# Kernel tuning notes

Measured on AMD Instinct MI355X. Metric: run time of the kernel, lower is better.

Reference implementation:

```python
import jax, jax.numpy as jnp
import numpy as np

MEM, KEY, VAL, DIN, BS, BQ = 1000, 64, 128, 512, 512, 65536


def setup_inputs() -> dict:
    key = jax.random.key(0)
    ks = jax.random.split(key, 20)

    def lin(k, fan_in, shape):
        return (jax.random.normal(k, shape, jnp.float32) / np.sqrt(fan_in)).astype(jnp.float32)

    return {
        "support_x": jax.random.normal(ks[0], (BS, DIN), jnp.float32),
        "support_y": jax.random.normal(ks[1], (BS, VAL), jnp.float32),
        "query_x": jax.random.normal(ks[2], (BQ, DIN), jnp.float32),
        "query_y": jax.random.normal(ks[3], (BQ, 1), jnp.float32),
        # base model: Linear(DIN -> KEY)
        "base_W": lin(ks[4], DIN, (DIN, KEY)),
        "base_b": jnp.zeros((KEY,), jnp.float32),
        # ExternalMemory projections
        "kp_W": lin(ks[5], KEY, (KEY, KEY)),
        "kp_b": jnp.zeros((KEY,), jnp.float32),
        "vp_W": lin(ks[6], VAL, (VAL, VAL)),
        "vp_b": jnp.zeros((VAL,), jnp.float32),
        # memory buffers (randn keys/values like register_buffer(torch.randn))
        "mem_keys": jax.random.normal(ks[7], (MEM, KEY), jnp.float32),
        "mem_values": jax.random.normal(ks[8], (MEM, VAL), jnp.float32),
        # ages: uniform so top-k picks distinct slots deterministically
        "mem_age": jax.random.uniform(ks[9], (MEM,), jnp.float32),
        # controller MLP: Linear(KEY+VAL,128) ReLU Linear(128,64) ReLU Linear(64,1)
        "c1_W": lin(ks[10], KEY + VAL, (KEY + VAL, 128)),
        "c1_b": jnp.zeros((128,), jnp.float32),
        "c2_W": lin(ks[11], 128, (128, 64)),
        "c2_b": jnp.zeros((64,), jnp.float32),
        "c3_W": lin(ks[12], 64, (64, 1)),
        "c3_b": jnp.zeros((1,), jnp.float32),
    }


def reference(support_x, support_y, query_x, query_y,
              base_W, base_b, kp_W, kp_b, vp_W, vp_b,
              mem_keys, mem_values, mem_age,
              c1_W, c1_b, c2_W, c2_b, c3_W, c3_b):
    # base model features
    support_feat = support_x @ base_W + base_b          # [BS, KEY]
    query_feat = query_x @ base_W + base_b              # [BQ, KEY]

    # --- memory.write(support_feat, support_y) ---
    proj_keys = support_feat @ kp_W + kp_b              # [BS, KEY]
    proj_vals = support_y @ vp_W + vp_b                 # [BS, VAL]
    _, oldest = jax.lax.top_k(mem_age, BS)              # evict oldest BS slots
    new_keys = mem_keys.at[oldest].set(proj_keys)       # [MEM, KEY]
    new_values = mem_values.at[oldest].set(proj_vals)   # [MEM, VAL]

    # --- memory.read(query_feat) ---
    proj_q = query_feat @ kp_W + kp_b                   # [BQ, KEY]
    sims = proj_q @ new_keys.T                          # [BQ, MEM]
    attn = jax.nn.softmax(sims, axis=-1)
    retrieved = attn @ new_values                       # [BQ, VAL]

    # --- controller MLP on [query_feat ; retrieved] ---
    aug = jnp.concatenate([query_feat, retrieved], axis=-1)  # [BQ, KEY+VAL]
    h = jax.nn.relu(aug @ c1_W + c1_b)
    h = jax.nn.relu(h @ c2_W + c2_b)
    query_pred = h @ c3_W + c3_b                        # [BQ, 1]

    meta_loss = jnp.mean((query_pred - query_y) ** 2)
    return meta_loss, query_pred, retrieved
```

## Files before the change

kernel.cpp:

```cpp
#include <hip/hip_runtime.h>

typedef _Float16 h8v __attribute__((ext_vector_type(8)));
typedef _Float16 h4v __attribute__((ext_vector_type(4)));
typedef float    f4v __attribute__((ext_vector_type(4)));

#define MFMA16(a,b,c) __builtin_amdgcn_mfma_f32_16x16x32_f16((a),(b),(c),0,0,0)
#define NEGF (-1e30f)

#define MEM 1000
#define KEY 64
#define VAL 128
#define DIN 512
#define BS  512
#define BQ  65536


typedef __attribute__((address_space(1))) const unsigned int guint;
typedef __attribute__((address_space(3))) unsigned int luint;

__device__ __forceinline__ void gld16(const _Float16* g, _Float16* l)
{
  __builtin_amdgcn_global_load_lds((guint*)g, (luint*)l, 16, 0, 0);
}

__device__ __forceinline__ h8v cvt8(const float* p)
{
  f4v u = *(const f4v*)p;
  f4v v = *(const f4v*)(p + 4);
  h8v a;
  a[0] = (_Float16)u.x; a[1] = (_Float16)u.y; a[2] = (_Float16)u.z; a[3] = (_Float16)u.w;
  a[4] = (_Float16)v.x; a[5] = (_Float16)v.y; a[6] = (_Float16)v.z; a[7] = (_Float16)v.w;
  return a;
}

__device__ __forceinline__ h8v cvt8nt(const float* p)
{
  f4v u = __builtin_nontemporal_load((const f4v*)p);
  f4v v = __builtin_nontemporal_load((const f4v*)(p + 4));
  h8v a;
  a[0] = (_Float16)u.x; a[1] = (_Float16)u.y; a[2] = (_Float16)u.z; a[3] = (_Float16)u.w;
  a[4] = (_Float16)v.x; a[5] = (_Float16)v.y; a[6] = (_Float16)v.z; a[7] = (_Float16)v.w;
  return a;
}

__global__ void k_prep1(const float* __restrict__ baseW, const float* __restrict__ base_b,
                        const float* __restrict__ kpW, const float* __restrict__ kp_b,
                        const float* __restrict__ vpW, const float* __restrict__ c1W,
                        const float* __restrict__ c2W, const float* __restrict__ age,
                        _Float16* __restrict__ WTf, float* __restrict__ bcomb,
                        _Float16* __restrict__ vpWt, _Float16* __restrict__ c1F,
                        _Float16* __restrict__ c2F, int* __restrict__ ranks,
                        float* __restrict__ out0)
{
  long id = (long)blockIdx.x * 256 + threadIdx.x;
  if (id < 65536) {
    int h = (int)id;
    int j = h & 7, lane = (h >> 3) & 63, KS = (h >> 9) & 15, F = h >> 13;
    int n = F * 16 + (lane & 15);
    int k = KS * 32 + ((lane >> 4) << 3) + j;
    float v;
    if (n < 64) v = baseW[(size_t)k * 64 + n];
    else {
      int nn = n - 64;
      const float* br = baseW + (size_t)k * 64;
      float s = 0.f;
      for (int t = 0; t < 64; ++t) s += br[t] * kpW[t * 64 + nn];
      v = s;
    }
    WTf[h] = (_Float16)v;
  } else if (id < 65664) {
    int i = (int)(id - 65536);
    if (i < 64) bcomb[i] = base_b[i];
    else {
      int n = i - 64;
      float s = kp_b[n];
      for (int t = 0; t < 64; ++t) s += base_b[t] * kpW[t * 64 + n];
      bcomb[i] = s;
    }
  } else if (id < 90240) {
    int h = (int)(id - 65664);
    int j = h & 7, lane = (h >> 3) & 63, KS = (h >> 9) % 6, F = (h >> 9) / 6;
    int n = F * 16 + (lane & 15);
    int k = KS * 32 + ((lane >> 4) << 3) + j;
    c1F[h] = (_Float16)c1W[(size_t)k * 128 + n];
  } else if (id < 98432) {
    int h = (int)(id - 90240);
    int j = h & 7, lane = (h >> 3) & 63, KS = (h >> 9) & 3, F = h >> 11;
    int n = F * 16 + (lane & 15);
    int k = KS * 32 + ((lane >> 4) << 3) + j;
    c2F[h] = (_Float16)c2W[(size_t)k * 64 + n];
  } else if (id < 114816) {
    long i = id - 98432;
    int n = (int)(i >> 7), k = (int)(i & 127);
    vpWt[i] = (_Float16)vpW[(size_t)k * 128 + n];
  } else if (id < 115816) {
    int jx = (int)(id - 114816);
    float aj = age[jx];
    int r = 0;
    for (int i2 = 0; i2 < MEM; ++i2) {
      float ai = age[i2];
      r += (ai > aj) || (ai == aj && i2 < jx);
    }
    ranks[jx] = r;
  } else if (id == 115816) {
    *out0 = 0.f;
  }
}

__global__ __launch_bounds__(64) void k_prep2(
    const float* __restrict__ sx, const float* __restrict__ sy,
    const _Float16* __restrict__ WTf, const float* __restrict__ bcomb,
    const _Float16* __restrict__ vpWt, const float* __restrict__ vp_b,
    float* __restrict__ pkeys, float* __restrict__ pvals)
{
  const int lane = threadIdx.x, quad = lane >> 4, l15 = lane & 15;
  const f4v fz = {0.f, 0.f, 0.f, 0.f};
  if (blockIdx.x < 32) {
    const int m0 = blockIdx.x * 16;
    f4v acc[4];
    #pragma unroll
    for (int f = 0; f < 4; ++f) acc[f] = fz;
    const float* xr = sx + (size_t)(m0 + l15) * DIN;
    #pragma unroll 4
    for (int ks = 0; ks < 16; ++ks) {
      int k0 = ks * 32 + quad * 8;
      h8v a = cvt8(xr + k0);
      #pragma unroll
      for (int f = 0; f < 4; ++f) {
        h8v b = *(const h8v*)(WTf + (size_t)((((4 + f) * 16) + ks) * 64 + lane) * 8);
        acc[f] = MFMA16(a, b, acc[f]);
      }
    }
    #pragma unroll
    for (int f = 0; f < 4; ++f) {
      int col = f * 16 + l15;
      float bb = bcomb[64 + col];
      #pragma unroll
      for (int r = 0; r < 4; ++r)
        pkeys[(size_t)(m0 + quad * 4 + r) * KEY + col] = acc[f][r] + bb;
    }
  } else {
    const int m0 = (blockIdx.x - 32) * 16;
    f4v acc[8];
    #pragma unroll
    for (int f = 0; f < 8; ++f) acc[f] = fz;
    const float* yr = sy + (size_t)(m0 + l15) * VAL;
    #pragma unroll
    for (int ks = 0; ks < 4; ++ks) {
      int k0 = ks * 32 + quad * 8;
      h8v a = cvt8(yr + k0);
      #pragma unroll
      for (int f = 0; f < 8; ++f) {
        h8v b = *(const h8v*)(vpWt + (size_t)(f * 16 + l15) * 128 + k0);
        acc[f] = MFMA16(a, b, acc[f]);
      }
    }
    #pragma unroll
    for (int f = 0; f < 8; ++f) {
      int col = f * 16 + l15;
      float bb = vp_b[col];
      #pragma unroll
      for (int r = 0; r < 4; ++r)
        pvals[(size_t)(m0 + quad * 4 + r) * VAL + col] = acc[f][r] + bb;
    }
  }
}

__global__ void k_prep3(const int* __restrict__ ranks, const float* __restrict__ pk,
                        const float* __restrict__ pv, const float* __restrict__ memK,
                        const float* __restrict__ memV,
                        _Float16* __restrict__ keysF, _Float16* __restrict__ valF)
{
  int id = blockIdx.x * 256 + threadIdx.x;
  if (id < 65536) {
    int j = id & 7, lane = (id >> 3) & 63, KS = (id >> 9) & 1, F = id >> 10;
    int n = F * 16 + (lane & 15);
    int k = KS * 32 + ((lane >> 4) << 3) + j;
    float v = 0.f;
    if (n < MEM) {
      int rk = ranks[n];
      v = (rk < BS) ? pk[(size_t)rk * KEY + k] : memK[(size_t)n * KEY + k];
    }
    keysF[id] = (_Float16)v;
  } else {
    int h = id - 65536;
    int j = h & 7, lane = (h >> 3) & 63, KS = (h >> 9) & 31, F = h >> 14;
    int nv = F * 16 + (lane & 15);
    int jm = KS * 32 + ((lane >> 4) << 3) + j;
    float v = 0.f;
    if (jm < MEM) {
      int rk = ranks[jm];
      v = (rk < BS) ? pv[(size_t)rk * VAL + nv] : memV[(size_t)jm * VAL + nv];
    }
    valF[h] = (_Float16)v;
  }
}

__global__ __launch_bounds__(512, 2) void k_fused(
    const float* __restrict__ qx, const float* __restrict__ qy,
    const _Float16* __restrict__ WTf, const float* __restrict__ bcomb,
    const float* __restrict__ c1_b, const float* __restrict__ c2_b,
    const float* __restrict__ c3W, const float* __restrict__ c3b,
    const _Float16* __restrict__ c1F, const _Float16* __restrict__ c2F,
    const _Float16* __restrict__ keysF, const _Float16* __restrict__ valF,
    float* __restrict__ dout)
{
  __shared__ __align__(16) char smem[151552];
  _Float16* const WTsh = (_Float16*)smem;
  _Float16* const K0   = (_Float16*)smem;
  _Float16* const K1   = (_Float16*)(smem + 16384);
  _Float16* const V0   = (_Float16*)(smem + 32768);
  _Float16* const V1   = (_Float16*)(smem + 65536);

  const int tid  = threadIdx.x;
  const int wid  = tid >> 6;
  const int lane = tid & 63;
  const int quad = lane >> 4;
  const int l15  = lane & 15;

  _Float16* const P_s  = (_Float16*)(smem + 98304 + wid * 6656);
  _Float16* const h2_s = P_s + 2176;

  const int tA  = blockIdx.x * 16 + wid * 2;
  const int q0A = tA * 16;
  const int q0B = q0A + 16;

  float* out_pred = dout + 1;
  float* out_ret  = dout + 1 + BQ;
  const f4v fz = {0.f, 0.f, 0.f, 0.f};

  #pragma unroll
  for (int i = 0; i < 16; ++i) {
    const int t = wid * 16 + i;
    gld16(WTf + (size_t)t * 512 + lane * 8, WTsh + t * 512);
  }
  asm volatile("s_waitcnt vmcnt(0)" ::: "memory");
  __syncthreads();

  f4v accA[8], accB[8];
  #pragma unroll
  for (int f = 0; f < 8; ++f) { accA[f] = fz; accB[f] = fz; }
  const float* xrA = qx + (size_t)(q0A + l15) * DIN;
  const float* xrB = qx + (size_t)(q0B + l15) * DIN;

  #pragma unroll 4
  for (int ks = 0; ks < 16; ++ks) {
    const int k0 = ks * 32 + quad * 8;
    h8v aA = cvt8nt(xrA + k0);
    h8v aB = cvt8nt(xrB + k0);
    #pragma unroll
    for (int f = 0; f < 8; ++f) {
      h8v b = *(const h8v*)(WTsh + (size_t)((f * 16 + ks) * 64 + lane) * 8);
      accA[f] = MFMA16(aA, b, accA[f]);
      accB[f] = MFMA16(aB, b, accB[f]);
    }
  }
  __syncthreads();

  _Float16* tbuf = (_Float16*)(smem + wid * 4352);
  h8v qf0A, qf1A, pq0A, pq1A, qf0B, qf1B, pq0B, pq1B;
  {
    #pragma unroll
    for (int f = 0; f < 8; ++f) {
      float bb = bcomb[f * 16 + l15];
      #pragma unroll
      for (int r = 0; r < 4; ++r)
        tbuf[(quad * 4 + r) * 136 + f * 16 + l15] = (_Float16)(accA[f][r] + bb);
    }
    qf0A = *(const h8v*)&tbuf[l15 * 136 +  0 + quad * 8];
    qf1A = *(const h8v*)&tbuf[l15 * 136 + 32 + quad * 8];
    pq0A = *(const h8v*)&tbuf[l15 * 136 + 64 + quad * 8];
    pq1A = *(const h8v*)&tbuf[l15 * 136 + 96 + quad * 8];
    #pragma unroll
    for (int f = 0; f < 8; ++f) {
      float bb = bcomb[f * 16 + l15];
      #pragma unroll
      for (int r = 0; r < 4; ++r)
        tbuf[(quad * 4 + r) * 136 + f * 16 + l15] = (_Float16)(accB[f][r] + bb);
    }
    qf0B = *(const h8v*)&tbuf[l15 * 136 +  0 + quad * 8];
    qf1B = *(const h8v*)&tbuf[l15 * 136 + 32 + quad * 8];
    pq0B = *(const h8v*)&tbuf[l15 * 136 + 64 + quad * 8];
    pq1B = *(const h8v*)&tbuf[l15 * 136 + 96 + quad * 8];
  }
  __syncthreads();

  #pragma unroll
  for (int i = 0; i < 2; ++i) {
    const int t = wid * 2 + i;
    gld16(keysF + (size_t)t * 512 + lane * 8, K0 + t * 512);
  }
  #pragma unroll
  for (int i = 0; i < 4; ++i) {
    const int t = wid * 4 + i;
    const int v = t >> 2, sub = t & 3;
    gld16(valF + ((size_t)(v * 32 + sub)) * 512 + lane * 8,
          V0 + (v * 4 + sub) * 512);
  }
  asm volatile("s_waitcnt vmcnt(0)" ::: "memory");
  __syncthreads();

  float rmA[4], rlA[4], rmB[4], rlB[4];
  #pragma unroll
  for (int r = 0; r < 4; ++r) { rmA[r] = NEGF; rlA[r] = 0.f; rmB[r] = NEGF; rlB[r] = 0.f; }
  f4v OA[8], OB[8];
  #pragma unroll
  for (int v = 0; v < 8; ++v) { OA[v] = fz; OB[v] = fz; }

  #pragma unroll 1
  for (int c = 0; c < 8; ++c) {
    const int cur = c & 1;
    _Float16* const Kc = cur ? K1 : K0;
    _Float16* const Vc = cur ? V1 : V0;
    _Float16* const Kn = cur ? K0 : K1;
    _Float16* const Vn = cur ? V0 : V1;

    if (c < 7) {
      const int nc = c + 1;
      const _Float16* kc = keysF + (size_t)nc * 8192;
      #pragma unroll
      for (int i = 0; i < 2; ++i) {
        const int t = wid * 2 + i;
        gld16(kc + (size_t)t * 512 + lane * 8, Kn + t * 512);
      }
      #pragma unroll
      for (int i = 0; i < 4; ++i) {
        const int t = wid * 4 + i;
        const int v = t >> 2, sub = t & 3;
        gld16(valF + ((size_t)(v * 32 + nc * 4 + sub)) * 512 + lane * 8,
              Vn + (v * 4 + sub) * 512);
      }
    } else {
      #pragma unroll
      for (int i = 0; i < 6; ++i) {
        const int t = wid * 6 + i;
        _Float16* dst = (t < 16) ? (K0 + t * 512) : (V0 + (t - 16) * 512);
        gld16(c1F + (size_t)t * 512 + lane * 8, dst);
      }
    }

    #pragma unroll
    for (int par = 0; par < 2; ++par) {
      const h8v p0 = par ? pq0B : pq0A;
      const h8v p1 = par ? pq1B : pq1A;
      float* rm = par ? rmB : rmA;
      float* rl = par ? rlB : rlA;
      f4v*   O  = par ? OB  : OA;

      f4v S[8];
      #pragma unroll
      for (int f = 0; f < 8; ++f) S[f] = fz;
      #pragma unroll
      for (int f = 0; f < 8; ++f) {
        h8v b0 = *(const h8v*)(Kc + (size_t)(f * 2 + 0) * 512 + lane * 8);
        h8v b1 = *(const h8v*)(Kc + (size_t)(f * 2 + 1) * 512 + lane * 8);
        S[f] = MFMA16(p0, b0, S[f]);
        S[f] = MFMA16(p1, b1, S[f]);
      }

      float cm[4] = {NEGF, NEGF, NEGF, NEGF};
      #pragma unroll
      for (int f = 0; f < 8; ++f) {
        const int col = c * 128 + f * 16 + l15;
        const bool ok = (col < MEM);
        #pragma unroll
        for (int r = 0; r < 4; ++r) {
          float s = ok ? S[f][r] : NEGF;
          S[f][r] = s;
          cm[r] = fmaxf(cm[r], s);
        }
      }
      #pragma unroll
      for (int r = 0; r < 4; ++r) {
        #pragma unroll
        for (int m = 1; m < 16; m <<= 1) cm[r] = fmaxf(cm[r], __shfl_xor(cm[r], m));
      }
      float al[4];
      #pragma unroll
      for (int r = 0; r < 4; ++r) {
        float mn = fmaxf(rm[r], cm[r]);
        al[r] = __expf(rm[r] - mn);
        rm[r] = mn;
      }
      float psl[4] = {0.f, 0.f, 0.f, 0.f};
      #pragma unroll
      for (int f = 0; f < 8; ++f)
        #pragma unroll
        for (int r = 0; r < 4; ++r) {
          float p = __expf(S[f][r] - rm[r]);
          S[f][r] = p;
          psl[r] += p;
        }
      #pragma unroll
      for (int r = 0; r < 4; ++r) rl[r] = rl[r] * al[r] + psl[r];

      #pragma unroll
      for (int f = 0; f < 8; ++f)
        #pragma unroll
        for (int r = 0; r < 4; ++r)
          P_s[(quad * 4 + r) * 136 + f * 16 + l15] = (_Float16)S[f][r];
      #pragma unroll
      for (int v = 0; v < 8; ++v)
        #pragma unroll
        for (int r = 0; r < 4; ++r) O[v][r] *= al[r];
      #pragma unroll
      for (int ks = 0; ks < 4; ++ks) {
        h8v a = *(const h8v*)&P_s[l15 * 136 + ks * 32 + quad * 8];
        #pragma unroll
        for (int v = 0; v < 8; ++v) {
          h8v b = *(const h8v*)(Vc + (size_t)(v * 4 + ks) * 512 + lane * 8);
          O[v] = MFMA16(a, b, O[v]);
        }
      }
    }

    asm volatile("s_waitcnt vmcnt(0)" ::: "memory");
    __syncthreads();
  }

  #pragma unroll
  for (int par = 0; par < 2; ++par) {
    const int q0 = par ? q0B : q0A;
    float* rl = par ? rlB : rlA;
    f4v*   O  = par ? OB  : OA;
    const h8v qf0 = par ? qf0B : qf0A;
    const h8v qf1 = par ? qf1B : qf1A;

    #pragma unroll
    for (int r = 0; r < 4; ++r) {
      #pragma unroll
      for (int m = 1; m < 16; m <<= 1) rl[r] += __shfl_xor(rl[r], m);
    }

    #pragma unroll
    for (int v = 0; v < 8; ++v)
      #pragma unroll
      for (int r = 0; r < 4; ++r)
        P_s[(quad * 4 + r) * 136 + v * 16 + l15] = (_Float16)(O[v][r] / rl[r]);

    #pragma unroll
    for (int it = 0; it < 8; ++it) {
      int flat = it * 256 + lane * 4;
      int row = flat >> 7, col = flat & 127;
      h4v t = *(const h4v*)&P_s[row * 136 + col];
      f4v o;
      o.x = (float)t[0]; o.y = (float)t[1]; o.z = (float)t[2]; o.w = (float)t[3];
      __builtin_nontemporal_store(o, (f4v*)(out_ret + (size_t)q0 * VAL + flat));
    }

    {
      f4v H[8];
      #pragma unroll
      for (int f = 0; f < 8; ++f) H[f] = fz;
      #pragma unroll
      for (int ks = 0; ks < 6; ++ks) {
        const int k0 = ks * 32;
        h8v a = (ks == 0) ? qf0 : (ks == 1) ? qf1
                 : *(const h8v*)&P_s[l15 * 136 + (k0 - 64) + quad * 8];
        #pragma unroll
        for (int f = 0; f < 8; ++f) {
          const int t = f * 6 + ks;
          const _Float16* bp = (t < 16) ? (K0 + (size_t)t * 512)
                                        : (V0 + (size_t)(t - 16) * 512);
          h8v b = *(const h8v*)(bp + lane * 8);
          H[f] = MFMA16(a, b, H[f]);
        }
      }
      #pragma unroll
      for (int f = 0; f < 8; ++f) {
        float bb = c1_b[f * 16 + l15];
        #pragma unroll
        for (int r = 0; r < 4; ++r)
          P_s[(quad * 4 + r) * 136 + f * 16 + l15] =
              (_Float16)fmaxf(0.f, H[f][r] + bb);
      }
    }

    {
      f4v G[4];
      #pragma unroll
      for (int f = 0; f < 4; ++f) G[f] = fz;
      #pragma unroll
      for (int ks = 0; ks < 4; ++ks) {
        h8v a = *(const h8v*)&P_s[l15 * 136 + ks * 32 + quad * 8];
        #pragma unroll
        for (int f = 0; f < 4; ++f) {
          h8v b = *(const h8v*)(c2F + (size_t)(f * 4 + ks) * 512 + lane * 8);
          G[f] = MFMA16(a, b, G[f]);
        }
      }
      #pragma unroll
      for (int f = 0; f < 4; ++f) {
        float bb = c2_b[f * 16 + l15];
        #pragma unroll
        for (int r = 0; r < 4; ++r)
          h2_s[(quad * 4 + r) * 72 + f * 16 + l15] =
              (_Float16)fmaxf(0.f, G[f][r] + bb);
      }
    }

    float lsum;
    {
      const int prow = lane >> 2, pj = lane & 3;
      float s = 0.f;
      #pragma unroll
      for (int k = 0; k < 16; ++k) {
        int kk = pj * 16 + k;
        s += (float)h2_s[prow * 72 + kk] * c3W[kk];
      }
      s += __shfl_xor(s, 1);
      s += __shfl_xor(s, 2);
      float pred = s + c3b[0];
      float diff = pred - qy[q0 + prow];
      if (pj == 0) out_pred[q0 + prow] = pred;
      lsum = diff * diff;
    }
    #pragma unroll
    for (int m = 1; m < 64; m <<= 1) lsum += __shfl_xor(lsum, m);
    if (lane == 0) atomicAdd(dout, lsum * (1.0f / (4.0f * (float)BQ)));
  }
}

extern "C" void kernel_launch(void* const* d_in, const int* in_sizes, int n_in,
                              void* d_out, int out_size, void* d_ws, size_t ws_size,
                              hipStream_t stream)
{
  const float* support_x = (const float*)d_in[0];
  const float* support_y = (const float*)d_in[1];
  const float* query_x   = (const float*)d_in[2];
  const float* query_y   = (const float*)d_in[3];
  const float* base_W    = (const float*)d_in[4];
  const float* base_b    = (const float*)d_in[5];
  const float* kp_W      = (const float*)d_in[6];
  const float* kp_b      = (const float*)d_in[7];
  const float* vp_W      = (const float*)d_in[8];
  const float* vp_b      = (const float*)d_in[9];
  const float* mem_keys  = (const float*)d_in[10];
  const float* mem_vals  = (const float*)d_in[11];
  const float* mem_age   = (const float*)d_in[12];
  const float* c1_W      = (const float*)d_in[13];
  const float* c1_b      = (const float*)d_in[14];
  const float* c2_W      = (const float*)d_in[15];
  const float* c2_b      = (const float*)d_in[16];
  const float* c3_W      = (const float*)d_in[17];
  const float* c3_b      = (const float*)d_in[18];

  char* w = (char*)d_ws;
  _Float16* WTf   = (_Float16*)(w + 0);
  _Float16* vpWt  = (_Float16*)(w + 131072);
  _Float16* c1F   = (_Float16*)(w + 163840);
  _Float16* c2F   = (_Float16*)(w + 212992);
  float*    bcomb = (float*)   (w + 229376);
  int*      ranks = (int*)     (w + 229888);
  float*    pkeys = (float*)   (w + 233984);
  float*    pvals = (float*)   (w + 365056);
  _Float16* keysF = (_Float16*)(w + 627200);
  _Float16* valF  = (_Float16*)(w + 758272);

  float* out = (float*)d_out;

  hipLaunchKernelGGL(k_prep1, dim3(453), dim3(256), 0, stream,
                     base_W, base_b, kp_W, kp_b, vp_W, c1_W, c2_W, mem_age,
                     WTf, bcomb, vpWt, c1F, c2F, ranks, out);
  hipLaunchKernelGGL(k_prep2, dim3(64), dim3(64), 0, stream,
                     support_x, support_y, WTf, bcomb, vpWt, vp_b, pkeys, pvals);
  hipLaunchKernelGGL(k_prep3, dim3(768), dim3(256), 0, stream,
                     ranks, pkeys, pvals, mem_keys, mem_vals, keysF, valF);
  hipLaunchKernelGGL(k_fused, dim3(BQ / 256), dim3(512), 0, stream,
                     query_x, query_y, WTf, bcomb, c1_b, c2_b, c3_W, c3_b,
                     c1F, c2F, keysF, valF, out);
}
```

Measured before the change: 377.7 us.

## Compute transposed scores and feed P to PV MFMA from registers

Swaps MFMA operand order so each lane holds the scores of one query row, which reduces the row max and sum reductions from 16-lane shuffles per register to two shuffles. The softmax probabilities are packed straight into the A operand of the PV MFMA instead of going through an LDS round trip, and the value buffer is permuted at prep time to match that k ordering. The per-row rescale factors are redistributed with shuffles. This removes LDS stores and loads and many cross-lane ops per chunk, at the cost of extra shuffles for the alpha and normaliser broadcast.

```diff
diff --git a/kernel.cpp b/kernel.cpp
--- a/kernel.cpp
+++ b/kernel.cpp
@@ -186,7 +186,7 @@
     int h = id - 65536;
     int j = h & 7, lane = (h >> 3) & 63, KS = (h >> 9) & 31, F = h >> 14;
     int nv = F * 16 + (lane & 15);
-    int jm = KS * 32 + ((lane >> 4) << 3) + j;
+    int jm = KS * 32 + ((j >> 2) << 4) + (((lane >> 4)) << 2) + (j & 3);
     float v = 0.f;
     if (jm < MEM) {
       int rk = ranks[jm];
@@ -195,6 +195,58 @@
     valF[h] = (_Float16)v;
   }
 }
+
+
+#define SM_PV(S, rm, rl, O, Vc, c)                                          \
+  {                                                                         \
+    float cm = NEGF;                                                        \
+    _Pragma("unroll")                                                       \
+    for (int f = 0; f < 8; ++f) {                                           \
+      const int sb = (c) * 128 + f * 16 + quad * 4;                         \
+      _Pragma("unroll")                                                     \
+      for (int r = 0; r < 4; ++r) {                                         \
+        float s = (sb + r < MEM) ? S[f][r] : NEGF;                          \
+        S[f][r] = s;                                                        \
+        cm = fmaxf(cm, s);                                                  \
+      }                                                                     \
+    }                                                                       \
+    cm = fmaxf(cm, __shfl_xor(cm, 16));                                     \
+    cm = fmaxf(cm, __shfl_xor(cm, 32));                                     \
+    float mn = fmaxf(rm, cm);                                               \
+    float al = __expf(rm - mn);                                             \
+    rm = mn;                                                                \
+    float psl = 0.f;                                                        \
+    _Pragma("unroll")                                                       \
+    for (int f = 0; f < 8; ++f)                                             \
+      _Pragma("unroll")                                                     \
+      for (int r = 0; r < 4; ++r) {                                         \
+        float p = __expf(S[f][r] - mn);                                     \
+        S[f][r] = p;                                                        \
+        psl += p;                                                           \
+      }                                                                     \
+    rl = rl * al + psl;                                                     \
+    float alO[4];                                                           \
+    _Pragma("unroll")                                                       \
+    for (int r = 0; r < 4; ++r) alO[r] = __shfl(al, quad * 4 + r);          \
+    _Pragma("unroll")                                                       \
+    for (int v = 0; v < 8; ++v)                                             \
+      _Pragma("unroll")                                                     \
+      for (int r = 0; r < 4; ++r) O[v][r] *= alO[r];                        \
+    _Pragma("unroll")                                                       \
+    for (int ks = 0; ks < 4; ++ks) {                                        \
+      h8v a;                                                                \
+      _Pragma("unroll")                                                     \
+      for (int e = 0; e < 4; ++e) {                                         \
+        a[e]     = (_Float16)S[2 * ks][e];                                  \
+        a[e + 4] = (_Float16)S[2 * ks + 1][e];                              \
+      }                                                                     \
+      _Pragma("unroll")                                                     \
+      for (int v = 0; v < 8; ++v) {                                         \
+        h8v b = *(const h8v*)(Vc + (size_t)(v * 4 + ks) * 512 + lane * 8);  \
+        O[v] = MFMA16(a, b, O[v]);                                          \
+      }                                                                     \
+    }                                                                       \
+  }
 
 __global__ __launch_bounds__(512, 2) void k_fused(
     const float* __restrict__ qx, const float* __restrict__ qy,
@@ -300,9 +352,7 @@
   asm volatile("s_waitcnt vmcnt(0)" ::: "memory");
   __syncthreads();
 
-  float rmA[4], rlA[4], rmB[4], rlB[4];
-  #pragma unroll
-  for (int r = 0; r < 4; ++r) { rmA[r] = NEGF; rlA[r] = 0.f; rmB[r] = NEGF; rlB[r] = 0.f; }
+  float rmA = NEGF, rlA = 0.f, rmB = NEGF, rlB = 0.f;
   f4v OA[8], OB[8];
   #pragma unroll
   for (int v = 0; v < 8; ++v) { OA[v] = fz; OB[v] = fz; }
@@ -339,104 +389,48 @@
       }
     }
 
-    #pragma unroll
-    for (int par = 0; par < 2; ++par) {
-      const h8v p0 = par ? pq0B : pq0A;
-      const h8v p1 = par ? pq1B : pq1A;
-      float* rm = par ? rmB : rmA;
-      float* rl = par ? rlB : rlA;
-      f4v*   O  = par ? OB  : OA;
-
-      f4v S[8];
-      #pragma unroll
-      for (int f = 0; f < 8; ++f) S[f] = fz;
-      #pragma unroll
-      for (int f = 0; f < 8; ++f) {
-        h8v b0 = *(const h8v*)(Kc + (size_t)(f * 2 + 0) * 512 + lane * 8);
-        h8v b1 = *(const h8v*)(Kc + (size_t)(f * 2 + 1) * 512 + lane * 8);
-        S[f] = MFMA16(p0, b0, S[f]);
-        S[f] = MFMA16(p1, b1, S[f]);
-      }
-
-      float cm[4] = {NEGF, NEGF, NEGF, NEGF};
-      #pragma unroll
-      for (int f = 0; f < 8; ++f) {
-        const int col = c * 128 + f * 16 + l15;
-        const bool ok = (col < MEM);
-        #pragma unroll
-        for (int r = 0; r < 4; ++r) {
-          float s = ok ? S[f][r] : NEGF;
-          S[f][r] = s;
-          cm[r] = fmaxf(cm[r], s);
-        }
-      }
-      #pragma unroll
-      for (int r = 0; r < 4; ++r) {
-        #pragma unroll
-        for (int m = 1; m < 16; m <<= 1) cm[r] = fmaxf(cm[r], __shfl_xor(cm[r], m));
-      }
-      float al[4];
-      #pragma unroll
-      for (int r = 0; r < 4; ++r) {
-        float mn = fmaxf(rm[r], cm[r]);
-        al[r] = __expf(rm[r] - mn);
-        rm[r] = mn;
-      }
-      float psl[4] = {0.f, 0.f, 0.f, 0.f};
-      #pragma unroll
-      for (int f = 0; f < 8; ++f)
-        #pragma unroll
-        for (int r = 0; r < 4; ++r) {
-          float p = __expf(S[f][r] - rm[r]);
-          S[f][r] = p;
-          psl[r] += p;
-        }
-      #pragma unroll
-      for (int r = 0; r < 4; ++r) rl[r] = rl[r] * al[r] + psl[r];
-
-      #pragma unroll
-      for (int f = 0; f < 8; ++f)
-        #pragma unroll
-        for (int r = 0; r < 4; ++r)
-          P_s[(quad * 4 + r) * 136 + f * 16 + l15] = (_Float16)S[f][r];
-      #pragma unroll
-      for (int v = 0; v < 8; ++v)
-        #pragma unroll
-        for (int r = 0; r < 4; ++r) O[v][r] *= al[r];
-      #pragma unroll
-      for (int ks = 0; ks < 4; ++ks) {
-        h8v a = *(const h8v*)&P_s[l15 * 136 + ks * 32 + quad * 8];
-        #pragma unroll
-        for (int v = 0; v < 8; ++v) {
-          h8v b = *(const h8v*)(Vc + (size_t)(v * 4 + ks) * 512 + lane * 8);
-          O[v] = MFMA16(a, b, O[v]);
-        }
-      }
-    }
+    f4v SA[8], SB[8];
+    #pragma unroll
+    for (int f = 0; f < 8; ++f) { SA[f] = fz; SB[f] = fz; }
+    #pragma unroll
+    for (int f = 0; f < 8; ++f) {
+      h8v b0 = *(const h8v*)(Kc + (size_t)(f * 2 + 0) * 512 + lane * 8);
+      h8v b1 = *(const h8v*)(Kc + (size_t)(f * 2 + 1) * 512 + lane * 8);
+      SA[f] = MFMA16(b0, pq0A, SA[f]);
+      SA[f] = MFMA16(b1, pq1A, SA[f]);
+      SB[f] = MFMA16(b0, pq0B, SB[f]);
+      SB[f] = MFMA16(b1, pq1B, SB[f]);
+    }
+
+    SM_PV(SA, rmA, rlA, OA, Vc, c)
+    SM_PV(SB, rmB, rlB, OB, Vc, c)
 
     asm volatile("s_waitcnt vmcnt(0)" ::: "memory");
     __syncthreads();
   }
 
+  rlA += __shfl_xor(rlA, 16); rlA += __shfl_xor(rlA, 32);
+  rlB += __shfl_xor(rlB, 16); rlB += __shfl_xor(rlB, 32);
+  float rlOA[4], rlOB[4];
+  #pragma unroll
+  for (int r = 0; r < 4; ++r) {
+    rlOA[r] = __shfl(rlA, quad * 4 + r);
+    rlOB[r] = __shfl(rlB, quad * 4 + r);
+  }
+
   #pragma unroll
   for (int par = 0; par < 2; ++par) {
     const int q0 = par ? q0B : q0A;
-    float* rl = par ? rlB : rlA;
-    f4v*   O  = par ? OB  : OA;
+    float* rlO = par ? rlOB : rlOA;
+    f4v*   O   = par ? OB  : OA;
     const h8v qf0 = par ? qf0B : qf0A;
     const h8v qf1 = par ? qf1B : qf1A;
 
     #pragma unroll
-    for (int r = 0; r < 4; ++r) {
-      #pragma unroll
-      for (int m = 1; m < 16; m <<= 1) rl[r] += __shfl_xor(rl[r], m);
-    }
-
-    #pragma unroll
     for (int v = 0; v < 8; ++v)
       #pragma unroll
       for (int r = 0; r < 4; ++r)
-        P_s[(quad * 4 + r) * 136 + v * 16 + l15] = (_Float16)(O[v][r] / rl[r]);
+        P_s[(quad * 4 + r) * 136 + v * 16 + l15] = (_Float16)(O[v][r] / rlO[r]);
 
     #pragma unroll
     for (int it = 0; it < 8; ++it) {
```

Result: no change. 383.1 us (+1.4%).
